# Kernel tuning notes

Measured on AMD Instinct MI355X. Metric: run time of the kernel, lower is better.

Reference implementation:

```python
import jax, jax.numpy as jnp
import numpy as np


def _haar_filters():
    # pywt 'haar': dec_lo = [s, s], dec_hi = [-s, s], s = 1/sqrt(2)
    s = np.float32(1.0 / np.sqrt(2.0))
    lo = np.array([s, s], dtype=np.float32)
    hi = np.array([-s, s], dtype=np.float32)
    # torch conv2d is cross-correlation; filter_2d = outer(row, col)
    # order matches module output concat: LL, LH, HL, HH
    f = np.stack([
        np.outer(lo, lo),  # LL
        np.outer(lo, hi),  # LH
        np.outer(hi, lo),  # HL
        np.outer(hi, hi),  # HH
    ]).astype(np.float32)  # (4, 2, 2)
    return jnp.asarray(f)


def setup_inputs() -> dict:
    key = jax.random.key(0)
    x = jax.random.normal(key, (8, 32, 512, 512), dtype=jnp.float32)
    return {"x": x, "filters": _haar_filters()}


def reference(x, filters):
    """Haar DWT2D: (B,C,H,W) -> (B,4C,H//2+1,W//2+1).

    Matches torch: pad to even dims (zeros), reflect-pad by 1,
    2x2 cross-correlation with stride 2 per subband, channel-concat
    [LL | LH | HL | HH].
    """
    b, c, h, w = x.shape
    pad_h = (2 - h % 2) % 2
    pad_w = (2 - w % 2) % 2
    if pad_h or pad_w:  # static shapes -> jit-safe Python branch
        x = jnp.pad(x, ((0, 0), (0, 0), (0, pad_h), (0, pad_w)))
    xp = jnp.pad(x, ((0, 0), (0, 0), (1, 1), (1, 1)), mode="reflect")
    # Stride-2 2x2 windows: tap (di,dj) of window (i,j) is xp[2i+di, 2j+dj].
    # xp has H+2 rows -> H//2 + 1 window rows (same for cols).
    x00 = xp[:, :, 0::2, 0::2]
    x01 = xp[:, :, 0::2, 1::2]
    x10 = xp[:, :, 1::2, 0::2]
    x11 = xp[:, :, 1::2, 1::2]
    win = jnp.stack([x00, x01, x10, x11], axis=-1)  # (B,C,h2,w2,4)
    f = filters.reshape(4, 4)                        # (subband, tap)
    out = jnp.einsum("bchwt,kt->bkchw", win, f)      # (B,4,C,h2,w2)
    b_, k_, c_, h2, w2 = out.shape
    return out.reshape(b_, k_ * c_, h2, w2)


if __name__ == "__main__":
    inp = setup_inputs()
    y = reference(**inp)
    print(y.shape, y.dtype)
```

## Files before the change

### kernel.cpp

```cpp
#include <hip/hip_runtime.h>


constexpr int H_IN  = 512;
constexpr int W_IN  = 512;
constexpr int H_OUT = 257;
constexpr int W_OUT = 257;
constexpr int C_IN  = 32;
constexpr int B_SZ  = 8;
constexpr long long PLANE_OUT = (long long)H_OUT * W_OUT;
constexpr long long PLANE_IN  = (long long)H_IN * W_IN;
constexpr long long TOTAL     = (long long)B_SZ * C_IN * PLANE_OUT;

__global__ __launch_bounds__(256)
void dwt2d_haar_kernel(const float* __restrict__ x,
                       const float* __restrict__ filt,
                       float* __restrict__ out) {
    long long idx = (long long)blockIdx.x * 256 + threadIdx.x;
    if (idx >= TOTAL) return;

    int bc  = (int)(idx / PLANE_OUT);
    int rem = (int)(idx - (long long)bc * PLANE_OUT);
    int i   = rem / W_OUT;
    int j   = rem - i * W_OUT;

    int r0 = 2 * i - 1; r0 = (r0 < 0)      ? 1          : r0;
    int r1 = 2 * i;     r1 = (r1 >= H_IN)  ? (H_IN - 2) : r1;
    int c0 = 2 * j - 1; c0 = (c0 < 0)      ? 1          : c0;
    int c1 = 2 * j;     c1 = (c1 >= W_IN)  ? (W_IN - 2) : c1;

    const float* xp = x + (long long)bc * PLANE_IN;
    float a = xp[(long long)r0 * W_IN + c0];
    float b = xp[(long long)r0 * W_IN + c1];
    float c = xp[(long long)r1 * W_IN + c0];
    float d = xp[(long long)r1 * W_IN + c1];

    float F[16];
#pragma unroll
    for (int t = 0; t < 16; ++t) F[t] = filt[t];

    int bb = bc >> 5;
    int cc = bc & 31;
    long long obase = ((long long)(bb * 128 + cc)) * PLANE_OUT + rem;
#pragma unroll
    for (int k = 0; k < 4; ++k) {
        float v = F[4 * k + 0] * a + F[4 * k + 1] * b
                + F[4 * k + 2] * c + F[4 * k + 3] * d;
        out[obase + (long long)(k * 32) * PLANE_OUT] = v;
    }
}

extern "C" void kernel_launch(void* const* d_in, const int* in_sizes, int n_in,
                              void* d_out, int out_size, void* d_ws, size_t ws_size,
                              hipStream_t stream) {
    const float* x    = (const float*)d_in[0];
    const float* filt = (const float*)d_in[1];
    float*       out  = (float*)d_out;

    long long grid = (TOTAL + 255) / 256;
    dwt2d_haar_kernel<<<(unsigned)grid, 256, 0, stream>>>(x, filt, out);
}
```

Before: 97.02 us.

## Restructure Haar DWT to one block per output row with LDS-staged float4 loads

Each block now handles one output row of one (batch, channel) plane. It loads the two needed input rows into shared memory with coalesced float4 reads, then computes the 257 outputs from LDS, writing with nontemporal stores. This replaces per-element 64-bit div/mod index math and strided scalar gathers from global memory. The cost is an extra barrier and a single thread handling the last column, which leaves that output serialized.

```diff
diff --git a/kernel.cpp b/kernel.cpp
--- a/kernel.cpp
+++ b/kernel.cpp
@@ -5,47 +5,63 @@
 constexpr int W_IN  = 512;
 constexpr int H_OUT = 257;
 constexpr int W_OUT = 257;
-constexpr int C_IN  = 32;
-constexpr int B_SZ  = 8;
 constexpr long long PLANE_OUT = (long long)H_OUT * W_OUT;
 constexpr long long PLANE_IN  = (long long)H_IN * W_IN;
-constexpr long long TOTAL     = (long long)B_SZ * C_IN * PLANE_OUT;
 
 __global__ __launch_bounds__(256)
-void dwt2d_haar_kernel(const float* __restrict__ x,
-                       const float* __restrict__ filt,
-                       float* __restrict__ out) {
-    long long idx = (long long)blockIdx.x * 256 + threadIdx.x;
-    if (idx >= TOTAL) return;
+void dwt2d_haar_rows(const float* __restrict__ x,
+                     const float* __restrict__ filt,
+                     float* __restrict__ out) {
+    const int i  = blockIdx.x;
+    const int bc = blockIdx.y;
+    const int t  = threadIdx.x;
 
-    int bc  = (int)(idx / PLANE_OUT);
-    int rem = (int)(idx - (long long)bc * PLANE_OUT);
-    int i   = rem / W_OUT;
-    int j   = rem - i * W_OUT;
+    __shared__ float row0[W_IN];
+    __shared__ float row1[W_IN];
 
-    int r0 = 2 * i - 1; r0 = (r0 < 0)      ? 1          : r0;
-    int r1 = 2 * i;     r1 = (r1 >= H_IN)  ? (H_IN - 2) : r1;
-    int c0 = 2 * j - 1; c0 = (c0 < 0)      ? 1          : c0;
-    int c1 = 2 * j;     c1 = (c1 >= W_IN)  ? (W_IN - 2) : c1;
+    int r0 = 2 * i - 1; if (r0 < 0)     r0 = 1;
+    int r1 = 2 * i;     if (r1 >= H_IN) r1 = H_IN - 2;
 
     const float* xp = x + (long long)bc * PLANE_IN;
-    float a = xp[(long long)r0 * W_IN + c0];
-    float b = xp[(long long)r0 * W_IN + c1];
-    float c = xp[(long long)r1 * W_IN + c0];
-    float d = xp[(long long)r1 * W_IN + c1];
+
+    {
+        const int half = t >> 7;
+        const int lane = (t & 127) << 2;
+        const float* src = xp + (long long)(half ? r1 : r0) * W_IN + lane;
+        float4 v = *reinterpret_cast<const float4*>(src);
+        float* dst = (half ? row1 : row0) + lane;
+        dst[0] = v.x; dst[1] = v.y; dst[2] = v.z; dst[3] = v.w;
+    }
+    __syncthreads();
 
     float F[16];
 #pragma unroll
-    for (int t = 0; t < 16; ++t) F[t] = filt[t];
+    for (int k = 0; k < 16; ++k) F[k] = filt[k];
 
-    int bb = bc >> 5;
-    int cc = bc & 31;
-    long long obase = ((long long)(bb * 128 + cc)) * PLANE_OUT + rem;
+    const int bb = bc >> 5;
+    const int cc = bc & 31;
+    const long long obase = (long long)(bb * 128 + cc) * PLANE_OUT
+                          + (long long)i * W_OUT;
+
+    {
+        int c0 = 2 * t - 1; if (c0 < 0) c0 = 1;
+        int c1 = 2 * t;
+        float a = row0[c0], b = row0[c1];
+        float c = row1[c0], d = row1[c1];
 #pragma unroll
-    for (int k = 0; k < 4; ++k) {
-        float v = F[4 * k + 0] * a + F[4 * k + 1] * b
-                + F[4 * k + 2] * c + F[4 * k + 3] * d;
-        out[obase + (long long)(k * 32) * PLANE_OUT] = v;
+        for (int k = 0; k < 4; ++k) {
+            float v = F[4*k+0] * a + F[4*k+1] * b + F[4*k+2] * c + F[4*k+3] * d;
+            __builtin_nontemporal_store(v, &out[obase + (long long)(k * 32) * PLANE_OUT + t]);
+        }
+    }
+    if (t == 0) {
+        float a = row0[511], b = row0[510];
+        float c = row1[511], d = row1[510];
+#pragma unroll
+        for (int k = 0; k < 4; ++k) {
+            float v = F[4*k+0] * a + F[4*k+1] * b + F[4*k+2] * c + F[4*k+3] * d;
+            __builtin_nontemporal_store(v, &out[obase + (long long)(k * 32) * PLANE_OUT + 256]);
+        }
     }
 }
 
@@ -56,6 +72,6 @@
     const float* filt = (const float*)d_in[1];
     float*       out  = (float*)d_out;
 
-    long long grid = (TOTAL + 255) / 256;
-    dwt2d_haar_kernel<<<(unsigned)grid, 256, 0, stream>>>(x, filt, out);
+    dim3 grid(H_OUT, 256);
+    dwt2d_haar_rows<<<grid, 256, 0, stream>>>(x, filt, out);
 }
```

Result: faster. 94.52 us (-2.6%).
